# Optimization experiments

Measured on AMD Instinct MI355X. Metric: run time of the kernel, lower is better.

Reference implementation:

```python
import jax, jax.numpy as jnp
import numpy as np

B, L, H = 128, 2048, 256


def setup_inputs() -> dict:
    key = jax.random.key(0)
    ks = jax.random.split(key, 9)
    s_in = 1.0 / np.sqrt(3.0)
    s_h = 1.0 / np.sqrt(H)
    return {
        "x": jax.random.normal(ks[0], (B, L, 3), dtype=jnp.float32),
        "Wp": jax.random.normal(ks[1], (3, H), dtype=jnp.float32) * s_in,
        "bp": jnp.zeros((H,), dtype=jnp.float32),
        "Wz": jax.random.normal(ks[2], (H, H), dtype=jnp.float32) * s_h,
        "bz": jnp.zeros((H,), dtype=jnp.float32),
        "Wh": jax.random.normal(ks[3], (H, H), dtype=jnp.float32) * s_h,
        "bh": jnp.zeros((H,), dtype=jnp.float32),
        "Wg": jax.random.normal(ks[4], (H, 1), dtype=jnp.float32) * s_h,
        "bg": jnp.zeros((1,), dtype=jnp.float32),
    }


def reference(x, Wp, bp, Wz, bz, Wh, bh, Wg, bg):
    # Precompute all per-timestep gate inputs with large batched GEMMs.
    inp = jnp.einsum("bli,ih->blh", x, Wp) + bp            # (B, L, H)
    z = jax.nn.sigmoid(jnp.einsum("blh,hk->blk", inp, Wz) + bz)   # update gate
    h_tilde = jnp.tanh(jnp.einsum("blh,hk->blk", inp, Wh) + bh)   # candidate

    # Sequential recurrence: h_t = (1 - z_t) * h_{t-1} + z_t * h_tilde_t.
    # pred_t = gauss_head(h_{t-1})  (pred is emitted BEFORE the state update).
    def step(h, zt_ht):
        zt, htl = zt_ht                      # each (B, H)
        pred = h @ Wg + bg                   # (B, 1) from previous state
        h_new = (1.0 - zt) * h + zt * htl
        return h_new, pred

    h0 = jnp.zeros((x.shape[0], Wz.shape[1]), dtype=x.dtype)
    zT = jnp.swapaxes(z, 0, 1)               # (L, B, H)
    hT = jnp.swapaxes(h_tilde, 0, 1)         # (L, B, H)
    _, preds = jax.lax.scan(step, h0, (zT, hT))
    preds = jnp.swapaxes(preds, 0, 1)        # (B, L, 1)
    return preds
```

## Files before the change

### kernel.cpp

```cpp
#include <hip/hip_runtime.h>

#define NB 128
#define NL 2048
#define NH 256
#define NSEG 16
#define SEGLEN (NL / NSEG)
#define RCHUNK 16
#define PBPITCH 9
#define CHUNK 32
#define NCHUNK (NL / CHUNK)
#define WORDS (CHUNK * 3)

typedef float f32x2 __attribute__((ext_vector_type(2)));
typedef __fp16 f16x2 __attribute__((ext_vector_type(2)));

__device__ __forceinline__ float fexp2(float v) { return __builtin_amdgcn_exp2f(v); }
__device__ __forceinline__ float frcp(float v)  { return __builtin_amdgcn_rcpf(v); }

__device__ __forceinline__ f32x2 pkfma(f32x2 a, f32x2 b, f32x2 c) {
#if __has_builtin(__builtin_elementwise_fma)
    return __builtin_elementwise_fma(a, b, c);
#else
    f32x2 r; r.x = fmaf(a.x, b.x, c.x); r.y = fmaf(a.y, b.y, c.y); return r;
#endif
}
__device__ __forceinline__ f32x2 splat2(float v) { f32x2 r; r.x = v; r.y = v; return r; }

union U32H2 { unsigned int u; f16x2 h; };

__global__ __launch_bounds__(256) void fold_kernel(
        const float* __restrict__ Wp, const float* __restrict__ bp,
        const float* __restrict__ Wz, const float* __restrict__ bz,
        const float* __restrict__ Wh, const float* __restrict__ bh,
        float* __restrict__ wsW) {
    const int tid = threadIdx.x;
    const int jj = tid & 63;
    const int hs = tid >> 6;
    const int j = blockIdx.x * 64 + jj;
    float mz0 = 0.f, mz1 = 0.f, mz2 = 0.f, cz = 0.f;
    float mh0 = 0.f, mh1 = 0.f, mh2 = 0.f, ch = 0.f;
#pragma unroll 8
    for (int i = 0; i < 64; ++i) {
        const int h = hs * 64 + i;
        const float wz = Wz[h * NH + j];
        const float wh = Wh[h * NH + j];
        const float p0 = Wp[h];
        const float p1 = Wp[NH + h];
        const float p2 = Wp[2 * NH + h];
        const float bb = bp[h];
        mz0 = fmaf(p0, wz, mz0); mz1 = fmaf(p1, wz, mz1); mz2 = fmaf(p2, wz, mz2);
        cz  = fmaf(bb, wz, cz);
        mh0 = fmaf(p0, wh, mh0); mh1 = fmaf(p1, wh, mh1); mh2 = fmaf(p2, wh, mh2);
        ch  = fmaf(bb, wh, ch);
    }
    __shared__ float red[256][9];
    red[tid][0] = mz0; red[tid][1] = mz1; red[tid][2] = mz2; red[tid][3] = cz;
    red[tid][4] = mh0; red[tid][5] = mh1; red[tid][6] = mh2; red[tid][7] = ch;
    __syncthreads();
    if (tid < 64) {
        float v[8];
#pragma unroll
        for (int k = 0; k < 8; ++k)
            v[k] = red[tid][k] + red[tid + 64][k] + red[tid + 128][k] + red[tid + 192][k];
        v[3] += bz[j];
        v[7] += bh[j];
        const float SZ = -1.4426950408889634f;
        const float SH = -2.8853900817779268f;
        float4* w4 = (float4*)(wsW + j * 8);
        w4[0] = make_float4(v[0] * SZ, v[1] * SZ, v[2] * SZ, v[3] * SZ);
        w4[1] = make_float4(v[4] * SH, v[5] * SH, v[6] * SH, v[7] * SH);
    }
}

#define GATE2(XQ, U0, AV, BV)                                                   \
    {                                                                           \
        const float* xf_ = (const float*)(XQ);                                  \
        f32x2 xx_ = { xf_[6*(U0)+0], xf_[6*(U0)+3] };                           \
        f32x2 xy_ = { xf_[6*(U0)+1], xf_[6*(U0)+4] };                           \
        f32x2 xz_ = { xf_[6*(U0)+2], xf_[6*(U0)+5] };                           \
        const f32x2 s1_ = pkfma(xx_, wax, pkfma(xy_, way, pkfma(xz_, waz, waw)));\
        const f32x2 s2_ = pkfma(xx_, wbx, pkfma(xy_, wby, pkfma(xz_, wbz, wbw)));\
        f32x2 e1_, e2_;                                                         \
        e1_.x = fexp2(s1_.x); e1_.y = fexp2(s1_.y);                             \
        e2_.x = fexp2(s2_.x); e2_.y = fexp2(s2_.y);                             \
        const f32x2 d2_ = e2_ + 1.f;                                            \
        const f32x2 e1d2_ = e1_ * d2_;                                          \
        const f32x2 dd_ = e1d2_ + d2_;                                          \
        const float rp_ = frcp(dd_.x * dd_.y);                                  \
        f32x2 rr_; rr_.x = dd_.y * rp_; rr_.y = dd_.x * rp_;                    \
        AV = e1d2_ * rr_;                                                       \
        BV = (1.f - e2_) * rr_;                                                 \
    }

#define LOAD8(XQ, SC)                                                           \
    _Pragma("unroll")                                                           \
    for (int i_ = 0; i_ < 6; ++i_) XQ[i_] = xs4[(SC) * 6 + i_];

__global__ __launch_bounds__(256, 4) void pass1_seg(
        const float* __restrict__ x, const float* __restrict__ wsW,
        float* __restrict__ Aarr, float* __restrict__ Barr) {
    const int tid = threadIdx.x;
    const int b = blockIdx.x >> 4;
    const int s = blockIdx.x & (NSEG - 1);

    const float4* wv = (const float4*)(wsW + tid * 8);
    const float4 wA4 = wv[0];
    const float4 wB4 = wv[1];
    const f32x2 wax = splat2(wA4.x), way = splat2(wA4.y), waz = splat2(wA4.z), waw = splat2(wA4.w);
    const f32x2 wbx = splat2(wB4.x), wby = splat2(wB4.y), wbz = splat2(wB4.z), wbw = splat2(wB4.w);

    const float4* xs4 = (const float4*)(x + ((size_t)b * NL + (size_t)s * SEGLEN) * 3);

#define P1_BODY(XQ)                                                             \
    _Pragma("unroll")                                                           \
    for (int u0 = 0; u0 < 4; ++u0) {                                            \
        f32x2 av, bv;                                                           \
        GATE2(XQ, u0, av, bv);                                                  \
        Bacc = fmaf(av.x, Bacc, bv.x);                                          \
        Bacc = fmaf(av.y, Bacc, bv.y);                                          \
        A *= av.x * av.y;                                                       \
    }

    float A = 1.f, Bacc = 0.f;
    float4 xa[6], xb[6];
    LOAD8(xa, 0);
    for (int c = 0; c < 8; ++c) {
        LOAD8(xb, 2 * c + 1);
        P1_BODY(xa);
        const int nxt = (c < 7) ? (2 * c + 2) : 0;
        LOAD8(xa, nxt);
        P1_BODY(xb);
    }
    const size_t o = ((size_t)b * NSEG + s) * NH + tid;
    Aarr[o] = A;
    Barr[o] = Bacc;
#undef P1_BODY
}

__global__ __launch_bounds__(256, 4) void pass3_pred(
        const float* __restrict__ x, const float* __restrict__ wsW,
        const float* __restrict__ Wg, const float* __restrict__ bg,
        const float* __restrict__ Aarr, const float* __restrict__ Barr,
        float* __restrict__ out) {
    const int tid = threadIdx.x;
    const int b = blockIdx.x >> 4;
    const int s = blockIdx.x & (NSEG - 1);

    const float4* wv = (const float4*)(wsW + tid * 8);
    const float4 wA4 = wv[0];
    const float4 wB4 = wv[1];
    const f32x2 wax = splat2(wA4.x), way = splat2(wA4.y), waz = splat2(wA4.z), waw = splat2(wA4.w);
    const f32x2 wbx = splat2(wB4.x), wby = splat2(wB4.y), wbz = splat2(wB4.z), wbw = splat2(wB4.w);
    const float wg = Wg[tid];
    const float bgv = bg[0];

    float h = 0.f;
    {
        const size_t pbase = (size_t)b * NSEG * NH + tid;
        for (int k0 = 0; k0 < NSEG; k0 += 8) {
            float Ak[8], Bk[8];
#pragma unroll
            for (int k = 0; k < 8; ++k) {
                const int kk = k0 + k;
                Ak[k] = (kk < s) ? Aarr[pbase + (size_t)kk * NH] : 1.f;
                Bk[k] = (kk < s) ? Barr[pbase + (size_t)kk * NH] : 0.f;
            }
#pragma unroll
            for (int k = 0; k < 8; ++k) h = fmaf(Ak[k], h, Bk[k]);
        }
    }

    const float4* xs4 = (const float4*)(x + ((size_t)b * NL + (size_t)s * SEGLEN) * 3);

    __shared__ unsigned int pbuf[NH * PBPITCH];
    __shared__ float part2[32][18];
    __shared__ float part3[4][17];

    const int q   = tid & 7;
    const int grp = tid >> 3;

#define P3_BODY(XQ, Q0)                                                         \
    _Pragma("unroll")                                                           \
    for (int u0 = 0; u0 < 4; ++u0) {                                            \
        f32x2 av, bv;                                                           \
        GATE2(XQ, u0, av, bv);                                                  \
        const float p0_ = h * wg;                \
        h = fmaf(av.x, h, bv.x);                                                \
        const float p1_ = h * wg;                                               \
        h = fmaf(av.y, h, bv.y);                                                \
        U32H2 pk_; pk_.h = __builtin_amdgcn_cvt_pkrtz(p0_, p1_);                \
        pk[(Q0) + u0] = pk_.u;                                                  \
    }

    float4 xa[6], xb[6];
    unsigned int pk[8];
    LOAD8(xa, 0);
    for (int c = 0; c < 8; ++c) {
        LOAD8(xb, 2 * c + 1);
        P3_BODY(xa, 0);
        const int nxt = (c < 7) ? (2 * c + 2) : 0;
        LOAD8(xa, nxt);
        P3_BODY(xb, 4);

#pragma unroll
        for (int v = 0; v < 8; ++v) pbuf[tid * PBPITCH + v] = pk[v];
        __syncthreads();
        f16x2 acc2 = (f16x2)0.f;
#pragma unroll
        for (int j = 0; j < 8; ++j) {
            const int c2 = grp * 8 + ((j + grp) & 7);
            U32H2 rd; rd.u = pbuf[c2 * PBPITCH + q];
            acc2 += rd.h;
        }
        {
            f32x2 pr; pr.x = (float)acc2.x; pr.y = (float)acc2.y;
            *(f32x2*)&part2[grp][2 * q] = pr;
        }
        __syncthreads();
        if (tid < 64) {
            const int t2 = tid & 15, quad = tid >> 4;
            float a3 = 0.f;
#pragma unroll
            for (int g2 = 0; g2 < 8; ++g2)
                a3 += part2[quad * 8 + g2][t2];
            part3[quad][t2] = a3;
            if (tid < 16) {
                const float o = part3[0][tid] + part3[1][tid]
                              + part3[2][tid] + part3[3][tid] + bgv;
                out[(size_t)b * NL + (size_t)s * SEGLEN + c * RCHUNK + tid] = o;
            }
        }
    }
#undef P3_BODY
}

__global__ __launch_bounds__(256) void scan_kernel_nows(
        const float* __restrict__ x, const float* __restrict__ wsW,
        const float* __restrict__ Wg, const float* __restrict__ bg,
        float* __restrict__ out) {
    const int tid  = threadIdx.x;
    const int lane = tid & 63;
    const int wid  = tid >> 6;
    const int b = blockIdx.x;

    const float4* wv = (const float4*)(wsW + tid * 8);
    const float4 wA = wv[0];
    const float4 wB = wv[1];
    const float  wg = Wg[tid];
    const float  bgv = bg[0];

    const float* xb = x + (size_t)b * (NL * 3);

    __shared__ float4 xbuf[2][CHUNK];
    __shared__ float  predbuf[2][4][CHUNK];
    float* xbf = (float*)xbuf;

    const int sw = tid;
    const int sidx = (sw / 3) * 4 + (sw % 3);

    if (tid < WORDS) xbf[sidx] = xb[sw];
    __syncthreads();

    float h = 0.f;
    for (int c = 0; c < NCHUNK; ++c) {
        const int cur = c & 1;
        float nv = 0.f;
        if (tid < WORDS && c + 1 < NCHUNK) nv = xb[(c + 1) * WORDS + sw];

        float p[CHUNK];
        const float4* xc = xbuf[cur];
#pragma unroll
        for (int t = 0; t < CHUNK; ++t) {
            const float4 xv = xc[t];
            const float e1 = fexp2(fmaf(xv.x, wA.x, fmaf(xv.y, wA.y, fmaf(xv.z, wA.z, wA.w))));
            const float e2 = fexp2(fmaf(xv.x, wB.x, fmaf(xv.y, wB.y, fmaf(xv.z, wB.z, wB.w))));
            const float d2 = 1.f + e2;
            const float e1d2 = e1 * d2;
            const float r  = frcp(e1d2 + d2);
            p[t] = h * wg;
            h = fmaf(e1d2 * r, h, (1.f - e2) * r);
        }
#pragma unroll
        for (int t = 0; t < CHUNK; ++t) {
            float v = p[t];
            v += __shfl_xor(v, 1, 64);
            v += __shfl_xor(v, 2, 64);
            v += __shfl_xor(v, 4, 64);
            v += __shfl_xor(v, 8, 64);
            v += __shfl_xor(v, 16, 64);
            v += __shfl_xor(v, 32, 64);
            p[t] = v;
        }
        if (lane == 0) {
            float4* dpr = (float4*)&predbuf[cur][wid][0];
#pragma unroll
            for (int j2 = 0; j2 < CHUNK / 4; ++j2)
                dpr[j2] = make_float4(p[4*j2], p[4*j2+1], p[4*j2+2], p[4*j2+3]);
        }
        if (tid < WORDS && c + 1 < NCHUNK) xbf[(cur ^ 1) * CHUNK * 4 + sidx] = nv;
        __syncthreads();
        if (tid < CHUNK) {
            const float ssum = predbuf[cur][0][tid] + predbuf[cur][1][tid]
                             + predbuf[cur][2][tid] + predbuf[cur][3][tid];
            out[(size_t)b * NL + c * CHUNK + tid] = ssum + bgv;
        }
    }
}

extern "C" void kernel_launch(void* const* d_in, const int* in_sizes, int n_in,
                              void* d_out, int out_size, void* d_ws, size_t ws_size,
                              hipStream_t stream) {
    const float* x  = (const float*)d_in[0];
    const float* Wp = (const float*)d_in[1];
    const float* bp = (const float*)d_in[2];
    const float* Wz = (const float*)d_in[3];
    const float* bz = (const float*)d_in[4];
    const float* Wh = (const float*)d_in[5];
    const float* bh = (const float*)d_in[6];
    const float* Wg = (const float*)d_in[7];
    const float* bg = (const float*)d_in[8];
    float* out = (float*)d_out;

    float* wsW = (float*)d_ws;

    fold_kernel<<<4, 256, 0, stream>>>(Wp, bp, Wz, bz, Wh, bh, wsW);

    const size_t need = (size_t)(8 * NH) * sizeof(float)
                      + (size_t)2 * NB * NSEG * NH * sizeof(float);
    if (ws_size >= need) {
        float* Aarr = wsW + 8 * NH;
        float* Barr = Aarr + (size_t)NB * NSEG * NH;
        pass1_seg<<<NB * NSEG, 256, 0, stream>>>(x, wsW, Aarr, Barr);
        pass3_pred<<<NB * NSEG, 256, 0, stream>>>(x, wsW, Wg, bg, Aarr, Barr, out);
    } else {
        scan_kernel_nows<<<NB, 256, 0, stream>>>(x, wsW, Wg, bg, out);
    }
}
```

Measured before the change: 76.75 us.

## Double prediction chunk size, halve barriers, simplify reduction, widen fold kernel grid

Measured after the change: 75.80 us. No clear change (-1.2%).

```diff
diff --git a/kernel.cpp b/kernel.cpp
--- a/kernel.cpp
+++ b/kernel.cpp
@@ -5,8 +5,8 @@
 #define NH 256
 #define NSEG 16
 #define SEGLEN (NL / NSEG)
-#define RCHUNK 16
-#define PBPITCH 9
+#define RCHUNK 32
+#define PBPITCH 17
 #define CHUNK 32
 #define NCHUNK (NL / CHUNK)
 #define WORDS (CHUNK * 3)
@@ -34,14 +34,14 @@
         const float* __restrict__ Wh, const float* __restrict__ bh,
         float* __restrict__ wsW) {
     const int tid = threadIdx.x;
-    const int jj = tid & 63;
-    const int hs = tid >> 6;
-    const int j = blockIdx.x * 64 + jj;
+    const int jj = tid & 15;
+    const int hs = tid >> 4;
+    const int j = blockIdx.x * 16 + jj;
     float mz0 = 0.f, mz1 = 0.f, mz2 = 0.f, cz = 0.f;
     float mh0 = 0.f, mh1 = 0.f, mh2 = 0.f, ch = 0.f;
-#pragma unroll 8
-    for (int i = 0; i < 64; ++i) {
-        const int h = hs * 64 + i;
+#pragma unroll
+    for (int i = 0; i < 16; ++i) {
+        const int h = hs * 16 + i;
         const float wz = Wz[h * NH + j];
         const float wh = Wh[h * NH + j];
         const float p0 = Wp[h];
@@ -57,11 +57,15 @@
     red[tid][0] = mz0; red[tid][1] = mz1; red[tid][2] = mz2; red[tid][3] = cz;
     red[tid][4] = mh0; red[tid][5] = mh1; red[tid][6] = mh2; red[tid][7] = ch;
     __syncthreads();
-    if (tid < 64) {
+    if (tid < 16) {
         float v[8];
 #pragma unroll
-        for (int k = 0; k < 8; ++k)
-            v[k] = red[tid][k] + red[tid + 64][k] + red[tid + 128][k] + red[tid + 192][k];
+        for (int k = 0; k < 8; ++k) {
+            float a = 0.f;
+#pragma unroll
+            for (int g = 0; g < 16; ++g) a += red[g * 16 + tid][k];
+            v[k] = a;
+        }
         v[3] += bz[j];
         v[7] += bh[j];
         const float SZ = -1.4426950408889634f;
@@ -84,12 +88,12 @@
         e1_.x = fexp2(s1_.x); e1_.y = fexp2(s1_.y);                             \
         e2_.x = fexp2(s2_.x); e2_.y = fexp2(s2_.y);                             \
         const f32x2 d2_ = e2_ + 1.f;                                            \
-        const f32x2 e1d2_ = e1_ * d2_;                                          \
-        const f32x2 dd_ = e1d2_ + d2_;                                          \
-        const float rp_ = frcp(dd_.x * dd_.y);                                  \
-        f32x2 rr_; rr_.x = dd_.y * rp_; rr_.y = dd_.x * rp_;                    \
-        AV = e1d2_ * rr_;                                                       \
-        BV = (1.f - e2_) * rr_;                                                 \
+        const f32x2 q_  = e1_ * d2_;                                            \
+        const f32x2 den_ = q_ + d2_;                               \
+        const float rp_ = frcp(den_.x * den_.y);                                \
+        f32x2 rr_; rr_.x = den_.y * rp_; rr_.y = den_.x * rp_;                  \
+        AV = q_ * rr_;                                          \
+        BV = (1.f - e2_) * rr_;                                 \
     }
 
 #define LOAD8(XQ, SC)                                                           \
@@ -162,8 +166,9 @@
 #pragma unroll
             for (int k = 0; k < 8; ++k) {
                 const int kk = k0 + k;
-                Ak[k] = (kk < s) ? Aarr[pbase + (size_t)kk * NH] : 1.f;
-                Bk[k] = (kk < s) ? Barr[pbase + (size_t)kk * NH] : 0.f;
+                const bool u = kk < s;
+                Ak[k] = u ? Aarr[pbase + (size_t)kk * NH] : 1.f;
+                Bk[k] = u ? Barr[pbase + (size_t)kk * NH] : 0.f;
             }
 #pragma unroll
             for (int k = 0; k < 8; ++k) h = fmaf(Ak[k], h, Bk[k]);
@@ -173,11 +178,10 @@
     const float4* xs4 = (const float4*)(x + ((size_t)b * NL + (size_t)s * SEGLEN) * 3);
 
     __shared__ unsigned int pbuf[NH * PBPITCH];
-    __shared__ float part2[32][18];
-    __shared__ float part3[4][17];
-
-    const int q   = tid & 7;
-    const int grp = tid >> 3;
+    __shared__ unsigned int part2[16 * PBPITCH];
+
+    const int q   = tid & 15;
+    const int grp = tid >> 4;
 
 #define P3_BODY(XQ, Q0)                                                         \
     _Pragma("unroll")                                                           \
@@ -189,46 +193,46 @@
         const float p1_ = h * wg;                                               \
         h = fmaf(av.y, h, bv.y);                                                \
         U32H2 pk_; pk_.h = __builtin_amdgcn_cvt_pkrtz(p0_, p1_);                \
-        pk[(Q0) + u0] = pk_.u;                                                  \
+        pbuf[tid * PBPITCH + (Q0) + u0] = pk_.u;                                \
     }
 
     float4 xa[6], xb[6];
-    unsigned int pk[8];
     LOAD8(xa, 0);
-    for (int c = 0; c < 8; ++c) {
-        LOAD8(xb, 2 * c + 1);
+    for (int c2 = 0; c2 < 4; ++c2) {
+        LOAD8(xb, 4 * c2 + 1);
         P3_BODY(xa, 0);
-        const int nxt = (c < 7) ? (2 * c + 2) : 0;
-        LOAD8(xa, nxt);
+        LOAD8(xa, 4 * c2 + 2);
         P3_BODY(xb, 4);
-
-#pragma unroll
-        for (int v = 0; v < 8; ++v) pbuf[tid * PBPITCH + v] = pk[v];
+        LOAD8(xb, 4 * c2 + 3);
+        P3_BODY(xa, 8);
+        {
+            const int nxt = (c2 < 3) ? (4 * c2 + 4) : 0;
+            LOAD8(xa, nxt);
+        }
+        P3_BODY(xb, 12);
         __syncthreads();
-        f16x2 acc2 = (f16x2)0.f;
-#pragma unroll
-        for (int j = 0; j < 8; ++j) {
-            const int c2 = grp * 8 + ((j + grp) & 7);
-            U32H2 rd; rd.u = pbuf[c2 * PBPITCH + q];
-            acc2 += rd.h;
-        }
         {
-            f32x2 pr; pr.x = (float)acc2.x; pr.y = (float)acc2.y;
-            *(f32x2*)&part2[grp][2 * q] = pr;
+            f16x2 acc2 = (f16x2)0.f;
+#pragma unroll
+            for (int j = 0; j < 16; ++j) {
+                U32H2 rd; rd.u = pbuf[(grp * 16 + j) * PBPITCH + q];
+                acc2 += rd.h;
+            }
+            U32H2 wr; wr.h = acc2;
+            part2[grp * PBPITCH + q] = wr.u;
         }
         __syncthreads();
-        if (tid < 64) {
-            const int t2 = tid & 15, quad = tid >> 4;
-            float a3 = 0.f;
-#pragma unroll
-            for (int g2 = 0; g2 < 8; ++g2)
-                a3 += part2[quad * 8 + g2][t2];
-            part3[quad][t2] = a3;
-            if (tid < 16) {
-                const float o = part3[0][tid] + part3[1][tid]
-                              + part3[2][tid] + part3[3][tid] + bgv;
-                out[(size_t)b * NL + (size_t)s * SEGLEN + c * RCHUNK + tid] = o;
+        if (tid < 16) {
+            f16x2 a3 = (f16x2)0.f;
+#pragma unroll
+            for (int g2 = 0; g2 < 16; ++g2) {
+                U32H2 rd; rd.u = part2[g2 * PBPITCH + tid];
+                a3 += rd.h;
             }
+            float2 o2;
+            o2.x = (float)a3.x + bgv;
+            o2.y = (float)a3.y + bgv;
+            *(float2*)&out[(size_t)b * NL + (size_t)s * SEGLEN + c2 * RCHUNK + 2 * tid] = o2;
         }
     }
 #undef P3_BODY
@@ -323,7 +327,7 @@
 
     float* wsW = (float*)d_ws;
 
-    fold_kernel<<<4, 256, 0, stream>>>(Wp, bp, Wz, bz, Wh, bh, wsW);
+    fold_kernel<<<16, 256, 0, stream>>>(Wp, bp, Wz, bz, Wh, bh, wsW);
 
     const size_t need = (size_t)(8 * NH) * sizeof(float)
                       + (size_t)2 * NB * NSEG * NH * sizeof(float);
```
